# Kernel tuning notes

Hardware: AMD Instinct MI355X
Metric: run time of the kernel (lower is better)

Reference implementation:

```python
import jax, jax.numpy as jnp
import numpy as np

B, S, D, F, E = 4, 1024, 768, 3072, 8


def setup_inputs() -> dict:
    key = jax.random.key(0)
    k0, k1, k2, k3 = jax.random.split(key, 4)
    hidden_states = jax.random.normal(k0, (B, S, D), dtype=jnp.float32)
    w_router = jax.random.normal(k1, (D, E), dtype=jnp.float32) * 0.02
    w1 = jax.random.normal(k2, (E, D, F), dtype=jnp.float32) * 0.02
    b1 = jnp.zeros((E, F), dtype=jnp.float32)
    w2 = jax.random.normal(k3, (E, F, D), dtype=jnp.float32) * 0.02
    b2 = jnp.zeros((E, D), dtype=jnp.float32)
    return {"hidden_states": hidden_states, "w_router": w_router,
            "w1": w1, "b1": b1, "w2": w2, "b2": b2}


def reference(hidden_states, w_router, w1, b1, w2, b2):
    # Switch-style top-1 router: logits -> softmax -> one-hot mask + max prob
    router_logits = jnp.einsum("bsd,de->bse", hidden_states, w_router)
    router_probs_full = jax.nn.softmax(router_logits, axis=-1)
    expert_index = jnp.argmax(router_probs_full, axis=-1)            # [B,S] int
    router_probs = jnp.max(router_probs_full, axis=-1, keepdims=True)  # [B,S,1]
    router_mask = jax.nn.one_hot(expert_index, E, dtype=hidden_states.dtype)  # [B,S,E]

    # Dispatch/compute/combine: each token goes to exactly one expert FFN.
    # Loop over the small fixed expert set (E=8), combine via the one-hot mask;
    # math is identical to the gather -> expert FFN -> scatter of the original.
    out = jnp.zeros_like(hidden_states)
    for e in range(E):
        h = jax.nn.relu(jnp.einsum("bsd,df->bsf", hidden_states, w1[e]) + b1[e])
        h = jnp.einsum("bsf,fd->bsd", h, w2[e]) + b2[e]
        out = out + router_mask[..., e:e + 1] * h

    hidden_out = router_probs * out  # scale by top-1 router prob, as in original
    return hidden_out, router_logits, expert_index
```

## Files before the change

### kernel.cpp

```cpp
#include <hip/hip_runtime.h>
#include <hip/hip_bf16.h>

#define T_TOK 4096
#define DIM   768
#define FF    3072
#define NE    8
#define MAXTILES 48

typedef __attribute__((ext_vector_type(8))) short bf16x8;
typedef __attribute__((ext_vector_type(4))) short bf16x4;
typedef __attribute__((ext_vector_type(4))) float f32x4;
typedef __attribute__((ext_vector_type(2))) float f32x2;

typedef __attribute__((address_space(1))) void gvoid_t;
typedef __attribute__((address_space(3))) void lvoid_t;

__device__ __forceinline__ void g2l16(const void* g, void* l) {
    __builtin_amdgcn_global_load_lds((gvoid_t*)(void*)g, (lvoid_t*)l, 16, 0, 0);
}

#define WAIT_VM0() __builtin_amdgcn_s_waitcnt(0x0F70)
#define WAIT_VM4() __builtin_amdgcn_s_waitcnt(0x0F74)
#define WAIT_VM6() __builtin_amdgcn_s_waitcnt(0x0F76)
#define RAW_BARRIER() asm volatile("s_barrier" ::: "memory")

__device__ __forceinline__ unsigned short f2bf(float f) {
    union { float f; unsigned int u; } v; v.f = f;
    unsigned int u = v.u;
    u += 0x7FFFu + ((u >> 16) & 1u);
    return (unsigned short)(u >> 16);
}

__device__ __forceinline__ bf16x8 pack8(f32x4 a, f32x4 b) {
    bf16x8 r;
    r[0] = (short)f2bf(a[0]); r[1] = (short)f2bf(a[1]);
    r[2] = (short)f2bf(a[2]); r[3] = (short)f2bf(a[3]);
    r[4] = (short)f2bf(b[0]); r[5] = (short)f2bf(b[1]);
    r[6] = (short)f2bf(b[2]); r[7] = (short)f2bf(b[3]);
    return r;
}

__global__ __launch_bounds__(256) void k_router(
    const float* __restrict__ x, const float* __restrict__ wr,
    float* __restrict__ out_logits, float* __restrict__ out_eidx,
    float* __restrict__ probs, int* __restrict__ eidx_i,
    int* __restrict__ counts, int* __restrict__ bucket,
    unsigned short* __restrict__ Xb, float* __restrict__ outh)
{
    int tok  = (blockIdx.x * 256 + threadIdx.x) >> 6;
    int lane = threadIdx.x & 63;
    if (tok >= T_TOK) return;
    {
        float* o = outh + (size_t)tok * DIM;
        #pragma unroll
        for (int j = 0; j < DIM / 256; j++)
            *(f32x4*)(o + j * 256 + lane * 4) = (f32x4)0.f;
    }
    const float* xr = x + (size_t)tok * DIM;
    unsigned short* xbr = Xb + (size_t)tok * DIM;
    float acc[NE];
    #pragma unroll
    for (int e = 0; e < NE; e++) acc[e] = 0.f;
    #pragma unroll
    for (int j = 0; j < DIM / 64; j++) {
        int d = j * 64 + lane;
        float xv = xr[d];
        xbr[d] = f2bf(xv);
        const float* wrow = wr + (size_t)d * NE;
        #pragma unroll
        for (int e = 0; e < NE; e++) acc[e] += xv * wrow[e];
    }
    #pragma unroll
    for (int e = 0; e < NE; e++) {
        #pragma unroll
        for (int off = 32; off >= 1; off >>= 1)
            acc[e] += __shfl_xor(acc[e], off);
    }
    if (lane == 0) {
        float mx = acc[0]; int mi = 0;
        #pragma unroll
        for (int e = 1; e < NE; e++) if (acc[e] > mx) { mx = acc[e]; mi = e; }
        float se = 0.f;
        #pragma unroll
        for (int e = 0; e < NE; e++) se += __expf(acc[e] - mx);
        #pragma unroll
        for (int e = 0; e < NE; e++) out_logits[(size_t)tok * NE + e] = acc[e];
        out_eidx[tok] = (float)mi;
        eidx_i[tok] = mi;
        probs[tok] = 1.f / se;
        int pos = atomicAdd(&counts[mi], 1);
        bucket[mi * T_TOK + pos] = tok;
    }
}

__global__ void k_compact(const int* __restrict__ counts, int* __restrict__ offsets,
                          int* __restrict__ bucket, int* __restrict__ sorted)
{
    __shared__ int soff[NE + 1];
    if (threadIdx.x == 0) {
        int s = 0;
        for (int e = 0; e < NE; e++) { soff[e] = s; s += counts[e]; }
        soff[NE] = s;
        for (int e = 0; e <= NE; e++) offsets[e] = soff[e];
    }
    __syncthreads();
    for (int e = 0; e < NE; e++) {
        int c = counts[e], o = soff[e];
        for (int i = threadIdx.x; i < c; i += blockDim.x)
            sorted[o + i] = bucket[e * T_TOK + i];
    }
    __syncthreads();
    if (threadIdx.x == 0) {
        int nt = 0;
        for (int e = 0; e < NE; e++) {
            int c = counts[e];
            for (int t = 0; t * 128 < c && nt < MAXTILES; t++)
                bucket[nt++] = (e << 8) | t;
        }
        for (int i = nt; i < MAXTILES; i++) bucket[i] = -1;
    }
}

__global__ __launch_bounds__(256) void k_tconv(
    const float* __restrict__ w1, unsigned short* __restrict__ wt1,
    const float* __restrict__ w2, unsigned short* __restrict__ wt2)
{
    int R, C, c0, r0;
    const float* in;
    unsigned short* out;
    if (blockIdx.z < NE) {
        R = DIM; C = FF;
        in  = w1  + (size_t)blockIdx.z * R * C;
        out = wt1 + (size_t)blockIdx.z * R * C;
        c0 = blockIdx.x * 64; r0 = blockIdx.y * 64;
    } else {
        R = FF; C = DIM;
        in  = w2  + (size_t)(blockIdx.z - NE) * R * C;
        out = wt2 + (size_t)(blockIdx.z - NE) * R * C;
        c0 = blockIdx.y * 64; r0 = blockIdx.x * 64;
    }
    __shared__ unsigned short t[64][72];
    const int tr = threadIdx.x >> 2, tc = (threadIdx.x & 3) * 16;
    const float* src = in + (size_t)(r0 + tr) * C + c0 + tc;
    f32x4 v0 = *(const f32x4*)(src);
    f32x4 v1 = *(const f32x4*)(src + 4);
    f32x4 v2 = *(const f32x4*)(src + 8);
    f32x4 v3 = *(const f32x4*)(src + 12);
    const int xb = (tc >> 4) & 3;
    const int pr = (((tr >> 3) ^ xb) & 7) * 8 + (tr & 7);
    #pragma unroll
    for (int j = 0; j < 4; j++) {
        t[tc + j][pr]      = f2bf(v0[j]);
        t[tc + 4 + j][pr]  = f2bf(v1[j]);
        t[tc + 8 + j][pr]  = f2bf(v2[j]);
        t[tc + 12 + j][pr] = f2bf(v3[j]);
    }
    __syncthreads();
    const int oc = threadIdx.x >> 2, orr = (threadIdx.x & 3) * 16;
    const int rx = (oc >> 4) & 3;
    const int p0 = ((((orr >> 3) + 0) ^ rx) & 7) * 8;
    const int p1 = ((((orr >> 3) + 1) ^ rx) & 7) * 8;
    bf16x8 o0 = *(const bf16x8*)&t[oc][p0];
    bf16x8 o1 = *(const bf16x8*)&t[oc][p1];
    unsigned short* dst = out + (size_t)(c0 + oc) * R + r0 + orr;
    *(bf16x8*)(dst)     = o0;
    *(bf16x8*)(dst + 8) = o1;
}

__global__ __launch_bounds__(256, 2) void k_gemm1(
    const unsigned short* __restrict__ Xb, const unsigned short* __restrict__ wt1,
    const float* __restrict__ b1, const int* __restrict__ sorted,
    const int* __restrict__ counts, const int* __restrict__ offsets,
    const int* __restrict__ tile_tab, unsigned short* __restrict__ Hbuf)
{
    const int tv = tile_tab[blockIdx.y];
    if (tv < 0) return;
    const int e  = tv >> 8;
    const int ti = tv & 255;
    const int cnt = counts[e];
    const int n0 = blockIdx.x * 256;
    const int off = offsets[e];
    const int rbase = ti * 128;
    const int tid = threadIdx.x, lane = tid & 63, wave = tid >> 6;
    const int wm = wave >> 1, wn = wave & 1;

    __shared__ unsigned short As[3][128][32];
    __shared__ unsigned short Bs[3][256][32];

    const int lr = lane >> 2;
    const int ls = (lane & 3) * 8;

    int r0 = rbase + wave * 32 + lr;        if (r0 >= cnt) r0 = rbase;
    int r1 = rbase + wave * 32 + 16 + lr;   if (r1 >= cnt) r1 = rbase;
    const unsigned short* aP0 = Xb + (size_t)sorted[off + r0] * DIM + ls;
    const unsigned short* aP1 = Xb + (size_t)sorted[off + r1] * DIM + ls;
    const unsigned short* wB  = wt1 + (size_t)e * FF * DIM;
    const unsigned short* bP0 = wB + (size_t)(n0 + wave * 64 +  0 + lr) * DIM + ls;
    const unsigned short* bP1 = wB + (size_t)(n0 + wave * 64 + 16 + lr) * DIM + ls;
    const unsigned short* bP2 = wB + (size_t)(n0 + wave * 64 + 32 + lr) * DIM + ls;
    const unsigned short* bP3 = wB + (size_t)(n0 + wave * 64 + 48 + lr) * DIM + ls;

    f32x4 acc[4][8];
    #pragma unroll
    for (int i = 0; i < 4; i++)
        #pragma unroll
        for (int j = 0; j < 8; j++) acc[i][j] = (f32x4)0.f;

    const int lrow = lane & 15, kq = lane >> 4;
    const int NIT = DIM / 32;

#define STAGE1(bufi, ko) do { \
    g2l16(aP0 + (ko), &As[bufi][wave * 32][0]);       \
    g2l16(aP1 + (ko), &As[bufi][wave * 32 + 16][0]);  \
    g2l16(bP0 + (ko), &Bs[bufi][wave * 64][0]);       \
    g2l16(bP1 + (ko), &Bs[bufi][wave * 64 + 16][0]);  \
    g2l16(bP2 + (ko), &Bs[bufi][wave * 64 + 32][0]);  \
    g2l16(bP3 + (ko), &Bs[bufi][wave * 64 + 48][0]);  \
} while (0)

    STAGE1(0, 0);
    __syncthreads();
    STAGE1(1, 32);

    for (int it = 0; it < NIT; ++it) {
        const int buf = it % 3;
        if (it > 0) {
            if (it + 1 < NIT) WAIT_VM6(); else WAIT_VM0();
            RAW_BARRIER();
        }
        if (it + 2 < NIT) {
            STAGE1((it + 2) % 3, (it + 2) * 32);
        }
        bf16x8 af[4], bfv[8];
        #pragma unroll
        for (int i = 0; i < 4; i++)
            af[i] = *(const bf16x8*)&As[buf][wm * 64 + i * 16 + lrow][kq * 8];
        #pragma unroll
        for (int j = 0; j < 8; j++)
            bfv[j] = *(const bf16x8*)&Bs[buf][wn * 128 + j * 16 + lrow][kq * 8];
        #pragma unroll
        for (int mi = 0; mi < 4; mi++)
            #pragma unroll
            for (int ni = 0; ni < 8; ni++)
                acc[mi][ni] = __builtin_amdgcn_mfma_f32_16x16x32_bf16(
                    af[mi], bfv[ni], acc[mi][ni], 0, 0, 0);
    }
#undef STAGE1

    const int quad = lane >> 4;
    #pragma unroll
    for (int ni = 0; ni < 8; ni++) {
        int gn = n0 + wn * 128 + ni * 16 + lrow;
        float bias = b1[e * FF + gn];
        #pragma unroll
        for (int mi = 0; mi < 4; mi++) {
            f32x4 v = acc[mi][ni];
            #pragma unroll
            for (int r = 0; r < 4; r++) {
                int ml = rbase + wm * 64 + mi * 16 + quad * 4 + r;
                if (ml < cnt) {
                    float h = v[r] + bias; h = h > 0.f ? h : 0.f;
                    Hbuf[(size_t)(off + ml) * FF + gn] = f2bf(h);
                }
            }
        }
    }
}

__global__ __launch_bounds__(256, 3) void k_gemm2(
    const unsigned short* __restrict__ Hbuf, const unsigned short* __restrict__ wt2,
    const float* __restrict__ b2, const int* __restrict__ sorted,
    const int* __restrict__ counts, const int* __restrict__ offsets,
    const int* __restrict__ tile_tab, const float* __restrict__ probs,
    float* __restrict__ outh)
{
    const int lid = blockIdx.x + 6 * blockIdx.y + 288 * blockIdx.z;
    const int xcd = lid & 7;
    const int j_  = lid >> 3;
    const int m   = j_ % 6;
    const int gg  = (j_ / 6) * 8 + xcd;
    const int by  = gg % MAXTILES;
    const int kc  = gg / MAXTILES;

    const int tv = tile_tab[by];
    if (tv < 0) return;
    const int e  = tv >> 8;
    const int ti = tv & 255;
    const int cnt = counts[e];
    const int n0 = m * 128;
    const int off = offsets[e];
    const int rbase = ti * 128;
    const int tid = threadIdx.x, lane = tid & 63, wave = tid >> 6;
    const int wm = wave >> 1, wn = wave & 1;

    __shared__ unsigned short As[3][128][32];
    __shared__ unsigned short Bs[3][128][32];
    __shared__ int   s_tok[128];
    __shared__ float s_prob[128];

    if (tid < 128) {
        int rr = rbase + tid; if (rr >= cnt) rr = rbase;
        int tk = sorted[off + rr];
        s_tok[tid]  = tk;
        s_prob[tid] = probs[tk];
    }

    const int lr = lane >> 2, ls = (lane & 3) * 8;
    int r0 = rbase + wave * 32 + lr;        if (r0 >= cnt) r0 = rbase;
    int r1 = rbase + wave * 32 + 16 + lr;   if (r1 >= cnt) r1 = rbase;
    const unsigned short* aP0 = Hbuf + (size_t)(off + r0) * FF + kc * 1024 + ls;
    const unsigned short* aP1 = Hbuf + (size_t)(off + r1) * FF + kc * 1024 + ls;
    const unsigned short* wB  = wt2 + (size_t)e * DIM * FF;
    const unsigned short* bP0 = wB + (size_t)(n0 + wave * 32 + lr) * FF + kc * 1024 + ls;
    const unsigned short* bP1 = wB + (size_t)(n0 + wave * 32 + 16 + lr) * FF + kc * 1024 + ls;

    f32x4 acc[4][4];
    #pragma unroll
    for (int i = 0; i < 4; i++)
        #pragma unroll
        for (int j = 0; j < 4; j++) acc[i][j] = (f32x4)0.f;

    const int lrow = lane & 15, kq = lane >> 4;
    const int NIT = 1024 / 32;

#define STAGE2(bufi, ko) do { \
    g2l16(aP0 + (ko), &As[bufi][wave * 32][0]);       \
    g2l16(aP1 + (ko), &As[bufi][wave * 32 + 16][0]);  \
    g2l16(bP0 + (ko), &Bs[bufi][wave * 32][0]);       \
    g2l16(bP1 + (ko), &Bs[bufi][wave * 32 + 16][0]);  \
} while (0)

    STAGE2(0, 0);
    __syncthreads();
    STAGE2(1, 32);

    for (int it = 0; it < NIT; ++it) {
        const int buf = it % 3;
        if (it > 0) {
            if (it + 1 < NIT) WAIT_VM4(); else WAIT_VM0();
            RAW_BARRIER();
        }
        if (it + 2 < NIT) {
            STAGE2((it + 2) % 3, (it + 2) * 32);
        }
        bf16x8 af[4], bfv[4];
        #pragma unroll
        for (int i = 0; i < 4; i++)
            af[i] = *(const bf16x8*)&As[buf][wm * 64 + i * 16 + lrow][kq * 8];
        #pragma unroll
        for (int i = 0; i < 4; i++)
            bfv[i] = *(const bf16x8*)&Bs[buf][wn * 64 + i * 16 + lrow][kq * 8];
        #pragma unroll
        for (int mi = 0; mi < 4; mi++)
            #pragma unroll
            for (int ni = 0; ni < 4; ni++)
                acc[mi][ni] = __builtin_amdgcn_mfma_f32_16x16x32_bf16(
                    af[mi], bfv[ni], acc[mi][ni], 0, 0, 0);
    }
#undef STAGE2

    const int quad = lane >> 4;
    #pragma unroll
    for (int ni = 0; ni < 4; ni++) {
        int gn = n0 + wn * 64 + ni * 16 + lrow;
        float bias = (kc == 0) ? b2[e * DIM + gn] : 0.f;
        #pragma unroll
        for (int mi = 0; mi < 4; mi++) {
            f32x4 v = acc[mi][ni];
            #pragma unroll
            for (int r = 0; r < 4; r++) {
                int mloc = wm * 64 + mi * 16 + quad * 4 + r;
                if (rbase + mloc < cnt) {
                    atomicAdd(&outh[(size_t)s_tok[mloc] * DIM + gn],
                              (v[r] + bias) * s_prob[mloc]);
                }
            }
        }
    }
}

__global__ __launch_bounds__(256) void k_gather_fb(
    const float* __restrict__ x, const int* __restrict__ sorted,
    unsigned short* __restrict__ Xg)
{
    int g0 = (blockIdx.x * 256 + threadIdx.x) * 8;
    if (g0 >= T_TOK * DIM) return;
    int row = g0 / DIM, col = g0 - row * DIM;
    const float* src = x + (size_t)sorted[row] * DIM + col;
    f32x4 a = *(const f32x4*)(src);
    f32x4 b = *(const f32x4*)(src + 4);
    *(bf16x8*)(Xg + (size_t)row * DIM + col) = pack8(a, b);
}

__global__ __launch_bounds__(256, 3) void k_gemm1_fb(
    const unsigned short* __restrict__ Xg, const float* __restrict__ w1,
    const float* __restrict__ b1, const int* __restrict__ counts,
    const int* __restrict__ offsets, unsigned short* __restrict__ Hbuf)
{
    const int e   = blockIdx.y >> 5;
    const int ti  = blockIdx.y & 31;
    const int cnt = counts[e];
    if (ti * 128 >= cnt) return;
    const int n0    = blockIdx.x * 128;
    const int off   = offsets[e];
    const int rbase = ti * 128;
    const int rmax  = cnt - rbase - 1;
    const int tid   = threadIdx.x;
    const int lane  = tid & 63;
    const int wave  = tid >> 6;
    const int wm = wave >> 1, wn = wave & 1;
    __shared__ unsigned short As[128][72];
    __shared__ unsigned short Bs[128][72];
    const float* w1e = w1 + (size_t)e * DIM * FF;
    f32x4 acc[4][4];
    #pragma unroll
    for (int i = 0; i < 4; i++)
        #pragma unroll
        for (int j = 0; j < 4; j++) acc[i][j] = (f32x4)0.f;
    const int arow = tid >> 1, aseg = tid & 1;
    const int are  = (arow <= rmax) ? arow : 0;
    const unsigned short* abase = Xg + (size_t)(off + rbase + are) * DIM + aseg * 32;
    const int kb = tid >> 5, nb = tid & 31;
    const float* bbase = w1e + (size_t)kb * 8 * FF + n0 + nb * 4;
    bf16x8 aR[4];
    f32x4  bR[8];
    #pragma unroll
    for (int j = 0; j < 4; j++) aR[j] = *(const bf16x8*)(abase + j * 8);
    #pragma unroll
    for (int r = 0; r < 8; r++) bR[r] = *(const f32x4*)(bbase + (size_t)r * FF);
    const int lrow = lane & 15, kq = lane >> 4;
    for (int it = 0; it < DIM / 64; ++it) {
        __syncthreads();
        #pragma unroll
        for (int j = 0; j < 4; j++)
            *(bf16x8*)&As[arow][aseg * 32 + j * 8] = aR[j];
        #pragma unroll
        for (int j = 0; j < 4; j++) {
            bf16x8 c;
            #pragma unroll
            for (int r = 0; r < 8; r++) c[r] = (short)f2bf(bR[r][j]);
            *(bf16x8*)&Bs[nb * 4 + j][kb * 8] = c;
        }
        __syncthreads();
        if (it + 1 < DIM / 64) {
            const unsigned short* an = abase + (it + 1) * 64;
            #pragma unroll
            for (int j = 0; j < 4; j++) aR[j] = *(const bf16x8*)(an + j * 8);
            const float* bn = bbase + (size_t)(it + 1) * 64 * FF;
            #pragma unroll
            for (int r = 0; r < 8; r++) bR[r] = *(const f32x4*)(bn + (size_t)r * FF);
        }
        #pragma unroll
        for (int ks = 0; ks < 2; ks++) {
            bf16x8 af[4], bfr[4];
            #pragma unroll
            for (int i = 0; i < 4; i++)
                af[i] = *(const bf16x8*)&As[wm * 64 + i * 16 + lrow][ks * 32 + kq * 8];
            #pragma unroll
            for (int i = 0; i < 4; i++)
                bfr[i] = *(const bf16x8*)&Bs[wn * 64 + i * 16 + lrow][ks * 32 + kq * 8];
            #pragma unroll
            for (int mi = 0; mi < 4; mi++)
                #pragma unroll
                for (int ni = 0; ni < 4; ni++)
                    acc[mi][ni] = __builtin_amdgcn_mfma_f32_16x16x32_bf16(
                        af[mi], bfr[ni], acc[mi][ni], 0, 0, 0);
        }
    }
    const int quad = lane >> 4;
    #pragma unroll
    for (int ni = 0; ni < 4; ni++) {
        int gn = n0 + wn * 64 + ni * 16 + lrow;
        float bias = b1[e * FF + gn];
        #pragma unroll
        for (int mi = 0; mi < 4; mi++) {
            f32x4 v = acc[mi][ni];
            #pragma unroll
            for (int r = 0; r < 4; r++) {
                int ml = wm * 64 + mi * 16 + quad * 4 + r;
                if (rbase + ml < cnt) {
                    float h = v[r] + bias;
                    h = h > 0.f ? h : 0.f;
                    Hbuf[(size_t)(off + rbase + ml) * FF + gn] = f2bf(h);
                }
            }
        }
    }
}

__global__ __launch_bounds__(256, 4) void k_gemm2_fb(
    const unsigned short* __restrict__ Hbuf, const float* __restrict__ w2,
    const float* __restrict__ b2, const int* __restrict__ sorted,
    const int* __restrict__ counts, const int* __restrict__ offsets,
    const float* __restrict__ probs, float* __restrict__ outh)
{
    const int e   = blockIdx.y >> 5;
    const int ti  = blockIdx.y & 31;
    const int cnt = counts[e];
    if (ti * 128 >= cnt) return;
    const int n0    = blockIdx.x * 64;
    const int off   = offsets[e];
    const int rbase = ti * 128;
    const int rmax  = cnt - rbase - 1;
    const int tid   = threadIdx.x;
    const int lane  = tid & 63;
    const int wave  = tid >> 6;
    const int wm = wave >> 1, wn = wave & 1;
    __shared__ unsigned short As[128][72];
    __shared__ unsigned short Bs[64][72];
    __shared__ int   s_tok[128];
    __shared__ float s_prob[128];
    if (tid < 128) {
        int r = rbase + tid;
        int tk = sorted[off + ((r < cnt) ? r : rbase)];
        s_tok[tid]  = tk;
        s_prob[tid] = probs[tk];
    }
    const float* w2e = w2 + (size_t)e * FF * DIM;
    f32x4 acc[4][2];
    #pragma unroll
    for (int i = 0; i < 4; i++)
        #pragma unroll
        for (int j = 0; j < 2; j++) acc[i][j] = (f32x4)0.f;
    const int arow = tid >> 1, aseg = tid & 1;
    const int are  = (arow <= rmax) ? arow : 0;
    const unsigned short* abase = Hbuf + (size_t)(off + rbase + are) * FF + aseg * 32;
    const int kb = tid >> 5, nb = tid & 31;
    const float* bbase = w2e + (size_t)kb * 8 * DIM + n0 + nb * 2;
    bf16x8 aR[4];
    f32x2  bR[8];
    #pragma unroll
    for (int j = 0; j < 4; j++) aR[j] = *(const bf16x8*)(abase + j * 8);
    #pragma unroll
    for (int r = 0; r < 8; r++) bR[r] = *(const f32x2*)(bbase + (size_t)r * DIM);
    const int lrow = lane & 15, kq = lane >> 4;
    for (int it = 0; it < FF / 64; ++it) {
        __syncthreads();
        #pragma unroll
        for (int j = 0; j < 4; j++)
            *(bf16x8*)&As[arow][aseg * 32 + j * 8] = aR[j];
        {
            bf16x8 c0, c1;
            #pragma unroll
            for (int r = 0; r < 8; r++) { c0[r] = (short)f2bf(bR[r][0]); c1[r] = (short)f2bf(bR[r][1]); }
            *(bf16x8*)&Bs[nb * 2 + 0][kb * 8] = c0;
            *(bf16x8*)&Bs[nb * 2 + 1][kb * 8] = c1;
        }
        __syncthreads();
        if (it + 1 < FF / 64) {
            const unsigned short* an = abase + (it + 1) * 64;
            #pragma unroll
            for (int j = 0; j < 4; j++) aR[j] = *(const bf16x8*)(an + j * 8);
            const float* bn = bbase + (size_t)(it + 1) * 64 * DIM;
            #pragma unroll
            for (int r = 0; r < 8; r++) bR[r] = *(const f32x2*)(bn + (size_t)r * DIM);
        }
        #pragma unroll
        for (int ks = 0; ks < 2; ks++) {
            bf16x8 af[4], bfr[2];
            #pragma unroll
            for (int i = 0; i < 4; i++)
                af[i] = *(const bf16x8*)&As[wm * 64 + i * 16 + lrow][ks * 32 + kq * 8];
            #pragma unroll
            for (int i = 0; i < 2; i++)
                bfr[i] = *(const bf16x8*)&Bs[wn * 32 + i * 16 + lrow][ks * 32 + kq * 8];
            #pragma unroll
            for (int mi = 0; mi < 4; mi++)
                #pragma unroll
                for (int ni = 0; ni < 2; ni++)
                    acc[mi][ni] = __builtin_amdgcn_mfma_f32_16x16x32_bf16(
                        af[mi], bfr[ni], acc[mi][ni], 0, 0, 0);
        }
    }
    const int quad = lane >> 4;
    #pragma unroll
    for (int ni = 0; ni < 2; ni++) {
        int gn = n0 + wn * 32 + ni * 16 + lrow;
        float bias = b2[e * DIM + gn];
        #pragma unroll
        for (int mi = 0; mi < 4; mi++) {
            f32x4 v = acc[mi][ni];
            #pragma unroll
            for (int r = 0; r < 4; r++) {
                int ml = wm * 64 + mi * 16 + quad * 4 + r;
                if (rbase + ml < cnt) {
                    outh[(size_t)s_tok[ml] * DIM + gn] = (v[r] + bias) * s_prob[ml];
                }
            }
        }
    }
}

extern "C" void kernel_launch(void* const* d_in, const int* in_sizes, int n_in,
                              void* d_out, int out_size, void* d_ws, size_t ws_size,
                              hipStream_t stream) {
    (void)in_sizes; (void)n_in; (void)out_size;
    const float* x  = (const float*)d_in[0];
    const float* wr = (const float*)d_in[1];
    const float* w1 = (const float*)d_in[2];
    const float* b1 = (const float*)d_in[3];
    const float* w2 = (const float*)d_in[4];
    const float* b2 = (const float*)d_in[5];

    float* out_hidden = (float*)d_out;
    float* out_logits = out_hidden + (size_t)T_TOK * DIM;
    float* out_eidx   = out_logits + (size_t)T_TOK * NE;

    char* ws = (char*)d_ws;
    int*   counts  = (int*)(ws + 0);
    int*   offsets = (int*)(ws + 64);
    float* probs   = (float*)(ws + 128);
    int*   eidx_i  = (int*)(ws + 16512);
    int*   sorted  = (int*)(ws + 32896);
    int*   bucket  = (int*)(ws + 49280);
    int*   tile_tab = bucket;
    unsigned short* Xb   = (unsigned short*)(ws + 180352);
    unsigned short* Hbuf = (unsigned short*)(ws + 6471808);
    unsigned short* wt1  = (unsigned short*)(ws + 31637632);
    unsigned short* wt2  = (unsigned short*)(ws + 69386368);
    const size_t NEED = 107135104;

    hipMemsetAsync(counts, 0, 32, stream);

    if (ws_size >= NEED) {
        k_router<<<dim3(T_TOK / 4), dim3(256), 0, stream>>>(
            x, wr, out_logits, out_eidx, probs, eidx_i, counts, bucket, Xb, out_hidden);
        k_compact<<<dim3(1), dim3(256), 0, stream>>>(counts, offsets, bucket, sorted);
        k_tconv<<<dim3(48, 12, 2 * NE), dim3(256), 0, stream>>>(w1, wt1, w2, wt2);
        k_gemm1<<<dim3(FF / 256, MAXTILES), dim3(256), 0, stream>>>(
            Xb, wt1, b1, sorted, counts, offsets, tile_tab, Hbuf);
        k_gemm2<<<dim3(DIM / 128, MAXTILES, 3), dim3(256), 0, stream>>>(
            Hbuf, wt2, b2, sorted, counts, offsets, tile_tab, probs, out_hidden);
    } else {
        k_router<<<dim3(T_TOK / 4), dim3(256), 0, stream>>>(
            x, wr, out_logits, out_eidx, probs, eidx_i, counts, bucket, Xb, out_hidden);
        k_compact<<<dim3(1), dim3(256), 0, stream>>>(counts, offsets, bucket, sorted);
        k_gather_fb<<<dim3(T_TOK * DIM / 8 / 256), dim3(256), 0, stream>>>(x, sorted, Xb);
        k_gemm1_fb<<<dim3(FF / 128, NE * 32), dim3(256), 0, stream>>>(
            Xb, w1, b1, counts, offsets, Hbuf);
        k_gemm2_fb<<<dim3(DIM / 64, NE * 32), dim3(256), 0, stream>>>(
            Hbuf, w2, b2, sorted, counts, offsets, probs, out_hidden);
    }
}
```

Measured before the change: 376.1 us.

## Use 8-wave blocks in both expert GEMMs with smaller per-wave tiles

Both grouped GEMM kernels now launch 512 threads (8 waves) per block instead of 256, keeping the same block tile. Each wave computes a smaller sub-tile (64x64 in gemm1, 32x64 in gemm2), which cuts accumulator registers per wave. The global-to-LDS loads are spread over more waves, and the vmcnt waits are adjusted to match. The aim is more resident waves to hide latency, at the cost of more LDS fragment reads per MFMA and possibly lower occupancy if the launch bounds cannot be met.

```diff
diff --git a/kernel.cpp b/kernel.cpp
--- a/kernel.cpp
+++ b/kernel.cpp
@@ -20,8 +20,8 @@
 }
 
 #define WAIT_VM0() __builtin_amdgcn_s_waitcnt(0x0F70)
-#define WAIT_VM4() __builtin_amdgcn_s_waitcnt(0x0F74)
-#define WAIT_VM6() __builtin_amdgcn_s_waitcnt(0x0F76)
+#define WAIT_VM2() __builtin_amdgcn_s_waitcnt(0x0F72)
+#define WAIT_VM3() __builtin_amdgcn_s_waitcnt(0x0F73)
 #define RAW_BARRIER() asm volatile("s_barrier" ::: "memory")
 
 __device__ __forceinline__ unsigned short f2bf(float f) {
@@ -167,7 +167,7 @@
     *(bf16x8*)(dst + 8) = o1;
 }
 
-__global__ __launch_bounds__(256, 2) void k_gemm1(
+__global__ __launch_bounds__(512, 4) void k_gemm1(
     const unsigned short* __restrict__ Xb, const unsigned short* __restrict__ wt1,
     const float* __restrict__ b1, const int* __restrict__ sorted,
     const int* __restrict__ counts, const int* __restrict__ offsets,
@@ -182,7 +182,7 @@
     const int off = offsets[e];
     const int rbase = ti * 128;
     const int tid = threadIdx.x, lane = tid & 63, wave = tid >> 6;
-    const int wm = wave >> 1, wn = wave & 1;
+    const int wm = wave >> 2, wn = wave & 3;
 
     __shared__ unsigned short As[3][128][32];
     __shared__ unsigned short Bs[3][256][32];
@@ -190,32 +190,38 @@
     const int lr = lane >> 2;
     const int ls = (lane & 3) * 8;
 
-    int r0 = rbase + wave * 32 + lr;        if (r0 >= cnt) r0 = rbase;
-    int r1 = rbase + wave * 32 + 16 + lr;   if (r1 >= cnt) r1 = rbase;
-    const unsigned short* aP0 = Xb + (size_t)sorted[off + r0] * DIM + ls;
-    const unsigned short* aP1 = Xb + (size_t)sorted[off + r1] * DIM + ls;
-    const unsigned short* wB  = wt1 + (size_t)e * FF * DIM;
-    const unsigned short* bP0 = wB + (size_t)(n0 + wave * 64 +  0 + lr) * DIM + ls;
-    const unsigned short* bP1 = wB + (size_t)(n0 + wave * 64 + 16 + lr) * DIM + ls;
-    const unsigned short* bP2 = wB + (size_t)(n0 + wave * 64 + 32 + lr) * DIM + ls;
-    const unsigned short* bP3 = wB + (size_t)(n0 + wave * 64 + 48 + lr) * DIM + ls;
-
-    f32x4 acc[4][8];
+    const unsigned short* wB = wt1 + (size_t)e * FF * DIM;
+    const unsigned short* gp[3];
+    unsigned short* lb[3];
+    int lstep[3];
+    #pragma unroll
+    for (int j = 0; j < 3; j++) {
+        int c = wave * 3 + j;
+        if (c < 8) {
+            int rr = rbase + c * 16 + lr; if (rr >= cnt) rr = rbase;
+            gp[j] = Xb + (size_t)sorted[off + rr] * DIM + ls;
+            lb[j] = &As[0][c * 16][0];
+            lstep[j] = 128 * 32;
+        } else {
+            gp[j] = wB + (size_t)(n0 + (c - 8) * 16 + lr) * DIM + ls;
+            lb[j] = &Bs[0][(c - 8) * 16][0];
+            lstep[j] = 256 * 32;
+        }
+    }
+
+    f32x4 acc[4][4];
     #pragma unroll
     for (int i = 0; i < 4; i++)
         #pragma unroll
-        for (int j = 0; j < 8; j++) acc[i][j] = (f32x4)0.f;
+        for (int j = 0; j < 4; j++) acc[i][j] = (f32x4)0.f;
 
     const int lrow = lane & 15, kq = lane >> 4;
     const int NIT = DIM / 32;
 
 #define STAGE1(bufi, ko) do { \
-    g2l16(aP0 + (ko), &As[bufi][wave * 32][0]);       \
-    g2l16(aP1 + (ko), &As[bufi][wave * 32 + 16][0]);  \
-    g2l16(bP0 + (ko), &Bs[bufi][wave * 64][0]);       \
-    g2l16(bP1 + (ko), &Bs[bufi][wave * 64 + 16][0]);  \
-    g2l16(bP2 + (ko), &Bs[bufi][wave * 64 + 32][0]);  \
-    g2l16(bP3 + (ko), &Bs[bufi][wave * 64 + 48][0]);  \
+    g2l16(gp[0] + (ko), lb[0] + (bufi) * lstep[0]); \
+    g2l16(gp[1] + (ko), lb[1] + (bufi) * lstep[1]); \
+    g2l16(gp[2] + (ko), lb[2] + (bufi) * lstep[2]); \
 } while (0)
 
     STAGE1(0, 0);
@@ -225,23 +231,23 @@
     for (int it = 0; it < NIT; ++it) {
         const int buf = it % 3;
         if (it > 0) {
-            if (it + 1 < NIT) WAIT_VM6(); else WAIT_VM0();
+            if (it + 1 < NIT) WAIT_VM3(); else WAIT_VM0();
             RAW_BARRIER();
         }
         if (it + 2 < NIT) {
             STAGE1((it + 2) % 3, (it + 2) * 32);
         }
-        bf16x8 af[4], bfv[8];
+        bf16x8 af[4], bfv[4];
         #pragma unroll
         for (int i = 0; i < 4; i++)
             af[i] = *(const bf16x8*)&As[buf][wm * 64 + i * 16 + lrow][kq * 8];
         #pragma unroll
-        for (int j = 0; j < 8; j++)
-            bfv[j] = *(const bf16x8*)&Bs[buf][wn * 128 + j * 16 + lrow][kq * 8];
+        for (int j = 0; j < 4; j++)
+            bfv[j] = *(const bf16x8*)&Bs[buf][wn * 64 + j * 16 + lrow][kq * 8];
         #pragma unroll
         for (int mi = 0; mi < 4; mi++)
             #pragma unroll
-            for (int ni = 0; ni < 8; ni++)
+            for (int ni = 0; ni < 4; ni++)
                 acc[mi][ni] = __builtin_amdgcn_mfma_f32_16x16x32_bf16(
                     af[mi], bfv[ni], acc[mi][ni], 0, 0, 0);
     }
@@ -249,8 +255,8 @@
 
     const int quad = lane >> 4;
     #pragma unroll
-    for (int ni = 0; ni < 8; ni++) {
-        int gn = n0 + wn * 128 + ni * 16 + lrow;
+    for (int ni = 0; ni < 4; ni++) {
+        int gn = n0 + wn * 64 + ni * 16 + lrow;
         float bias = b1[e * FF + gn];
         #pragma unroll
         for (int mi = 0; mi < 4; mi++) {
@@ -267,7 +273,7 @@
     }
 }
 
-__global__ __launch_bounds__(256, 3) void k_gemm2(
+__global__ __launch_bounds__(512, 6) void k_gemm2(
     const unsigned short* __restrict__ Hbuf, const unsigned short* __restrict__ wt2,
     const float* __restrict__ b2, const int* __restrict__ sorted,
     const int* __restrict__ counts, const int* __restrict__ offsets,
@@ -306,17 +312,27 @@
     }
 
     const int lr = lane >> 2, ls = (lane & 3) * 8;
-    int r0 = rbase + wave * 32 + lr;        if (r0 >= cnt) r0 = rbase;
-    int r1 = rbase + wave * 32 + 16 + lr;   if (r1 >= cnt) r1 = rbase;
-    const unsigned short* aP0 = Hbuf + (size_t)(off + r0) * FF + kc * 1024 + ls;
-    const unsigned short* aP1 = Hbuf + (size_t)(off + r1) * FF + kc * 1024 + ls;
-    const unsigned short* wB  = wt2 + (size_t)e * DIM * FF;
-    const unsigned short* bP0 = wB + (size_t)(n0 + wave * 32 + lr) * FF + kc * 1024 + ls;
-    const unsigned short* bP1 = wB + (size_t)(n0 + wave * 32 + 16 + lr) * FF + kc * 1024 + ls;
-
-    f32x4 acc[4][4];
-    #pragma unroll
-    for (int i = 0; i < 4; i++)
+
+    const unsigned short* wB = wt2 + (size_t)e * DIM * FF;
+    const unsigned short* gp[2];
+    unsigned short* lb[2];
+    #pragma unroll
+    for (int j = 0; j < 2; j++) {
+        int c = wave * 2 + j;
+        if (c < 8) {
+            int rr = rbase + c * 16 + lr; if (rr >= cnt) rr = rbase;
+            gp[j] = Hbuf + (size_t)(off + rr) * FF + kc * 1024 + ls;
+            lb[j] = &As[0][c * 16][0];
+        } else {
+            gp[j] = wB + (size_t)(n0 + (c - 8) * 16 + lr) * FF + kc * 1024 + ls;
+            lb[j] = &Bs[0][(c - 8) * 16][0];
+        }
+    }
+    const int lstep = 128 * 32;
+
+    f32x4 acc[2][4];
+    #pragma unroll
+    for (int i = 0; i < 2; i++)
         #pragma unroll
         for (int j = 0; j < 4; j++) acc[i][j] = (f32x4)0.f;
 
@@ -324,10 +340,8 @@
     const int NIT = 1024 / 32;
 
 #define STAGE2(bufi, ko) do { \
-    g2l16(aP0 + (ko), &As[bufi][wave * 32][0]);       \
-    g2l16(aP1 + (ko), &As[bufi][wave * 32 + 16][0]);  \
-    g2l16(bP0 + (ko), &Bs[bufi][wave * 32][0]);       \
-    g2l16(bP1 + (ko), &Bs[bufi][wave * 32 + 16][0]);  \
+    g2l16(gp[0] + (ko), lb[0] + (bufi) * lstep); \
+    g2l16(gp[1] + (ko), lb[1] + (bufi) * lstep); \
 } while (0)
 
     STAGE2(0, 0);
@@ -337,21 +351,21 @@
     for (int it = 0; it < NIT; ++it) {
         const int buf = it % 3;
         if (it > 0) {
-            if (it + 1 < NIT) WAIT_VM4(); else WAIT_VM0();
+            if (it + 1 < NIT) WAIT_VM2(); else WAIT_VM0();
             RAW_BARRIER();
         }
         if (it + 2 < NIT) {
             STAGE2((it + 2) % 3, (it + 2) * 32);
         }
-        bf16x8 af[4], bfv[4];
-        #pragma unroll
-        for (int i = 0; i < 4; i++)
-            af[i] = *(const bf16x8*)&As[buf][wm * 64 + i * 16 + lrow][kq * 8];
-        #pragma unroll
-        for (int i = 0; i < 4; i++)
-            bfv[i] = *(const bf16x8*)&Bs[buf][wn * 64 + i * 16 + lrow][kq * 8];
-        #pragma unroll
-        for (int mi = 0; mi < 4; mi++)
+        bf16x8 af[2], bfv[4];
+        #pragma unroll
+        for (int i = 0; i < 2; i++)
+            af[i] = *(const bf16x8*)&As[buf][wm * 32 + i * 16 + lrow][kq * 8];
+        #pragma unroll
+        for (int j = 0; j < 4; j++)
+            bfv[j] = *(const bf16x8*)&Bs[buf][wn * 64 + j * 16 + lrow][kq * 8];
+        #pragma unroll
+        for (int mi = 0; mi < 2; mi++)
             #pragma unroll
             for (int ni = 0; ni < 4; ni++)
                 acc[mi][ni] = __builtin_amdgcn_mfma_f32_16x16x32_bf16(
@@ -365,11 +379,11 @@
         int gn = n0 + wn * 64 + ni * 16 + lrow;
         float bias = (kc == 0) ? b2[e * DIM + gn] : 0.f;
         #pragma unroll
-        for (int mi = 0; mi < 4; mi++) {
+        for (int mi = 0; mi < 2; mi++) {
             f32x4 v = acc[mi][ni];
             #pragma unroll
             for (int r = 0; r < 4; r++) {
-                int mloc = wm * 64 + mi * 16 + quad * 4 + r;
+                int mloc = wm * 32 + mi * 16 + quad * 4 + r;
                 if (rbase + mloc < cnt) {
                     atomicAdd(&outh[(size_t)s_tok[mloc] * DIM + gn],
                               (v[r] + bias) * s_prob[mloc]);
@@ -627,9 +641,9 @@
             x, wr, out_logits, out_eidx, probs, eidx_i, counts, bucket, Xb, out_hidden);
         k_compact<<<dim3(1), dim3(256), 0, stream>>>(counts, offsets, bucket, sorted);
         k_tconv<<<dim3(48, 12, 2 * NE), dim3(256), 0, stream>>>(w1, wt1, w2, wt2);
-        k_gemm1<<<dim3(FF / 256, MAXTILES), dim3(256), 0, stream>>>(
+        k_gemm1<<<dim3(FF / 256, MAXTILES), dim3(512), 0, stream>>>(
             Xb, wt1, b1, sorted, counts, offsets, tile_tab, Hbuf);
-        k_gemm2<<<dim3(DIM / 128, MAXTILES, 3), dim3(256), 0, stream>>>(
+        k_gemm2<<<dim3(DIM / 128, MAXTILES, 3), dim3(512), 0, stream>>>(
             Hbuf, wt2, b2, sorted, counts, offsets, tile_tab, probs, out_hidden);
     } else {
         k_router<<<dim3(T_TOK / 4), dim3(256), 0, stream>>>(
```

Result: faster. 357.5 us (-4.9%).
